# Kernel tuning notes

Measured on AMD Instinct MI355X. Metric: run time of the kernel, lower is better.

Reference implementation:

```python
import jax, jax.numpy as jnp
import numpy as np

N_NODES = 50000
N_EDGES = 800000
IN_FEATS = 128
NUM_HEADS = 4
OUT_FEATS = 32


def setup_inputs() -> dict:
    key = jax.random.key(0)
    k1, k2, k3, k4 = jax.random.split(key, 4)
    feat = jax.random.normal(k1, (N_NODES, IN_FEATS), dtype=jnp.float32)
    # nn.Linear weight: [out_features, in_features] = [H*D, in]
    W = jax.random.normal(k2, (NUM_HEADS * OUT_FEATS, IN_FEATS), dtype=jnp.float32) * (1.0 / np.sqrt(IN_FEATS))
    src = jax.random.randint(k3, (N_EDGES,), 0, N_NODES, dtype=jnp.int32)
    dst = jax.random.randint(k4, (N_EDGES,), 0, N_NODES, dtype=jnp.int32)
    return {"feat": feat, "W": W, "src": src, "dst": dst}


def reference(feat, W, src, dst):
    N = feat.shape[0]
    H, D = NUM_HEADS, OUT_FEATS
    scale = jnp.float32(1.0 / np.sqrt(D))
    # fc: feat @ W.T  ->  [N, H, D]
    ft = (feat @ W.T).reshape(N, H, D)
    ft_src = ft[src]                                   # [E, H, D] gather
    # u_dot_v: per-edge, per-head dot product, scaled by sqrt(out_feats)
    a = jnp.einsum('ehd,ehd->eh', ft_src, ft[dst]) * scale  # [E, H]
    # edge softmax normalized by destination node (numerically stable)
    m = jax.ops.segment_max(a, dst, num_segments=N)    # [N, H]
    e = jnp.exp(a - m[dst])                            # [E, H]
    s = jax.ops.segment_sum(e, dst, num_segments=N)    # [N, H]
    sa = e / s[dst]                                    # [E, H]
    # u_mul_e + sum aggregation: scatter-add weighted source features into dst
    out = jax.ops.segment_sum(ft_src * sa[:, :, None], dst, num_segments=N)  # [N, H, D]
    return out
```

## Files before the change

kernel.cpp:

```cpp
#include <hip/hip_runtime.h>
#include <math.h>

#define NN 50000
#define NE 800000
#define HH 4
#define DD 32

typedef __attribute__((ext_vector_type(8))) short short8;
typedef __attribute__((ext_vector_type(4))) float f32x4;

__device__ __forceinline__ unsigned short f2bf(float x) {
    unsigned u = __float_as_uint(x);
    unsigned r = (u + 0x7FFF + ((u >> 16) & 1)) >> 16;
    return (unsigned short)r;
}

__device__ __forceinline__ short8 pack8(float4 p, float4 q) {
    short8 r;
    r[0] = (short)f2bf(p.x); r[1] = (short)f2bf(p.y);
    r[2] = (short)f2bf(p.z); r[3] = (short)f2bf(p.w);
    r[4] = (short)f2bf(q.x); r[5] = (short)f2bf(q.y);
    r[6] = (short)f2bf(q.z); r[7] = (short)f2bf(q.w);
    return r;
}

__global__ __launch_bounds__(256) void k_gemm(const float* __restrict__ feat,
                                              const float* __restrict__ W,
                                              float* __restrict__ ft, int N) {
    __shared__ short8 wlds[2048];

    int tid = threadIdx.x;
#pragma unroll
    for (int j = 0; j < 8; ++j) {
        int f = tid + j * 256;
        int kc = f >> 9, ct = (f >> 6) & 7, l = f & 63;
        int o = ct * 16 + (l & 15);
        int kb = kc * 32 + ((l >> 4) << 3);
        const float* wp = W + o * 128 + kb;
        float4 p = *(const float4*)wp;
        float4 q = *(const float4*)(wp + 4);
        wlds[f] = pack8(p, q);
    }
    __syncthreads();

    int l = tid & 63;
    int w = tid >> 6;
    int row0 = blockIdx.x * 64;
    int arow = row0 + w * 16 + (l & 15);
    bool valid = arow < N;
    const float* fb = feat + (size_t)(valid ? arow : 0) * 128 + ((l >> 4) << 3);

    f32x4 acc[8];
#pragma unroll
    for (int ct = 0; ct < 8; ++ct) acc[ct] = (f32x4){0.f, 0.f, 0.f, 0.f};

#pragma unroll
    for (int kc = 0; kc < 4; ++kc) {
        short8 a;
        if (valid) {
            float4 p = *(const float4*)(fb + kc * 32);
            float4 q = *(const float4*)(fb + kc * 32 + 4);
            a = pack8(p, q);
        } else {
            a = (short8){0, 0, 0, 0, 0, 0, 0, 0};
        }
#pragma unroll
        for (int ct = 0; ct < 8; ++ct) {
            short8 b = wlds[kc * 512 + ct * 64 + l];
            acc[ct] = __builtin_amdgcn_mfma_f32_16x16x32_bf16(a, b, acc[ct], 0, 0, 0);
        }
    }

    int oc = l & 15;
    int rg = l >> 4;
#pragma unroll
    for (int i = 0; i < 4; ++i) {
        int r = row0 + w * 16 + rg * 4 + i;
        if (r < N) {
            float* op = ft + (size_t)r * 128 + oc;
#pragma unroll
            for (int ct = 0; ct < 8; ++ct) op[ct * 16] = acc[ct][i];
        }
    }
}

__global__ __launch_bounds__(256) void k_hist(const int* __restrict__ dst, int* __restrict__ cnt) {
    int e = blockIdx.x * 256 + threadIdx.x;
    if (e < NE) atomicAdd(&cnt[dst[e]], 1);
}

__global__ __launch_bounds__(256) void k_scan1(const int* __restrict__ cnt, int* __restrict__ row,
                                               int* __restrict__ partial, int n) {
    __shared__ int sh[256];
    int i = blockIdx.x * 256 + threadIdx.x;
    int x = (i < n) ? cnt[i] : 0;
    sh[threadIdx.x] = x;
    __syncthreads();
    for (int off = 1; off < 256; off <<= 1) {
        int v = (threadIdx.x >= off) ? sh[threadIdx.x - off] : 0;
        __syncthreads();
        sh[threadIdx.x] += v;
        __syncthreads();
    }
    if (i < n) row[i] = sh[threadIdx.x] - x;
    if (threadIdx.x == 255) partial[blockIdx.x] = sh[255];
}

__global__ __launch_bounds__(256) void k_scan2(int* __restrict__ partial, int nb) {
    __shared__ int sh[256];
    int t = threadIdx.x;
    int x = (t < nb) ? partial[t] : 0;
    sh[t] = x;
    __syncthreads();
    for (int off = 1; off < 256; off <<= 1) {
        int v = (t >= off) ? sh[t - off] : 0;
        __syncthreads();
        sh[t] += v;
        __syncthreads();
    }
    if (t < nb) partial[t] = sh[t] - x;
}

__global__ __launch_bounds__(256) void k_scan3(int* __restrict__ row, int* __restrict__ cur,
                                               const int* __restrict__ partial, int n) {
    int i = blockIdx.x * 256 + threadIdx.x;
    if (i < n) {
        int val = row[i] + partial[blockIdx.x];
        row[i] = val;
        cur[i] = val;
    }
    if (i == 0) row[n] = NE;
}

__global__ __launch_bounds__(256) void k_fill(const int* __restrict__ src, const int* __restrict__ dst,
                                              int* __restrict__ cur, int* __restrict__ srcs) {
    int e = blockIdx.x * 256 + threadIdx.x;
    if (e >= NE) return;
    int p = atomicAdd(&cur[dst[e]], 1);
    srcs[p] = src[e];
}

__global__ __launch_bounds__(256) void k_agg(const float2* __restrict__ ft2,
                                             const int* __restrict__ row,
                                             const int* __restrict__ srcs,
                                             float2* __restrict__ out2) {
    int n = blockIdx.x * 4 + (threadIdx.x >> 6);
    int l = threadIdx.x & 63;
    int r0 = row[n], r1 = row[n + 1];
    size_t base = (size_t)n * 64 + l;
    float2 fd = ft2[base];
    float m = -INFINITY, s = 0.f;
    float ax = 0.f, ay = 0.f;
    int p = r0;
    for (; p + 1 < r1; p += 2) {
        int s0 = srcs[p], s1 = srcs[p + 1];
        float2 f0 = ft2[(size_t)s0 * 64 + l];
        float2 f1 = ft2[(size_t)s1 * 64 + l];
        float v0 = fd.x * f0.x + fd.y * f0.y;
        float v1 = fd.x * f1.x + fd.y * f1.y;
        v0 += __shfl_xor(v0, 1);  v1 += __shfl_xor(v1, 1);
        v0 += __shfl_xor(v0, 2);  v1 += __shfl_xor(v1, 2);
        v0 += __shfl_xor(v0, 4);  v1 += __shfl_xor(v1, 4);
        v0 += __shfl_xor(v0, 8);  v1 += __shfl_xor(v1, 8);
        v0 *= 0.17677669529663687f;
        v1 *= 0.17677669529663687f;
        float mn = fmaxf(fmaxf(m, v0), v1);
        float sc = __expf(m - mn);
        float w0 = __expf(v0 - mn);
        float w1 = __expf(v1 - mn);
        s = s * sc + w0 + w1;
        ax = ax * sc + w0 * f0.x + w1 * f1.x;
        ay = ay * sc + w0 * f0.y + w1 * f1.y;
        m = mn;
    }
    if (p < r1) {
        int s0 = srcs[p];
        float2 f0 = ft2[(size_t)s0 * 64 + l];
        float v0 = fd.x * f0.x + fd.y * f0.y;
        v0 += __shfl_xor(v0, 1);
        v0 += __shfl_xor(v0, 2);
        v0 += __shfl_xor(v0, 4);
        v0 += __shfl_xor(v0, 8);
        v0 *= 0.17677669529663687f;
        float mn = fmaxf(m, v0);
        float sc = __expf(m - mn);
        float w0 = __expf(v0 - mn);
        s = s * sc + w0;
        ax = ax * sc + w0 * f0.x;
        ay = ay * sc + w0 * f0.y;
    }
    float inv = (r1 > r0) ? 1.f / s : 0.f;
    out2[base] = make_float2(ax * inv, ay * inv);
}

extern "C" void kernel_launch(void* const* d_in, const int* in_sizes, int n_in,
                              void* d_out, int out_size, void* d_ws, size_t ws_size,
                              hipStream_t stream) {
    const float* feat = (const float*)d_in[0];
    const float* W    = (const float*)d_in[1];
    const int*   src  = (const int*)d_in[2];
    const int*   dst  = (const int*)d_in[3];
    float* out = (float*)d_out;

    float* ft   = (float*)d_ws;
    int*   row  = (int*)(ft + (size_t)NN * 128);
    int*   cur  = row + (NN + 1);
    int*   srcs = cur + NN;
    int*   cnt  = srcs + NE;
    int*   part = cnt + NN;

    const int NB1 = (NN + 255) / 256;

    hipMemsetAsync(cnt, 0, (size_t)NN * sizeof(int), stream);
    k_hist<<<(NE + 255) / 256, 256, 0, stream>>>(dst, cnt);
    k_scan1<<<NB1, 256, 0, stream>>>(cnt, row, part, NN);
    k_scan2<<<1, 256, 0, stream>>>(part, NB1);
    k_scan3<<<NB1, 256, 0, stream>>>(row, cur, part, NN);
    k_fill<<<(NE + 255) / 256, 256, 0, stream>>>(src, dst, cur, srcs);

    k_gemm<<<(NN + 63) / 64, 256, 0, stream>>>(feat, W, ft, NN);
    k_agg<<<NN / 4, 256, 0, stream>>>((const float2*)ft, row, srcs, (float2*)out);
}
```

Before: 260.0 us.

## Fuse CSR build into one cooperative kernel with grid syncs

Replaces the five CSR-construction launches (histogram, three scan stages, fill) with a single cooperative kernel that uses grid-wide syncs between phases. The histogram's atomic return value is stored per edge as a position, so the fill phase writes directly to row[dst]+pos without a second atomic pass. The aim is to remove launch overhead and the second round of contended atomics. In exchange it adds an extra NE-sized workspace array and grid-sync costs, and it depends on all 2048 blocks being co-resident.

```diff
diff --git a/kernel.cpp b/kernel.cpp
--- a/kernel.cpp
+++ b/kernel.cpp
@@ -1,5 +1,8 @@
 #include <hip/hip_runtime.h>
+#include <hip/hip_cooperative_groups.h>
 #include <math.h>
+
+namespace cg = cooperative_groups;
 
 #define NN 50000
 #define NE 800000
@@ -84,60 +87,63 @@
     }
 }
 
-__global__ __launch_bounds__(256) void k_hist(const int* __restrict__ dst, int* __restrict__ cnt) {
-    int e = blockIdx.x * 256 + threadIdx.x;
-    if (e < NE) atomicAdd(&cnt[dst[e]], 1);
-}
-
-__global__ __launch_bounds__(256) void k_scan1(const int* __restrict__ cnt, int* __restrict__ row,
-                                               int* __restrict__ partial, int n) {
+__global__ __launch_bounds__(256, 8) void k_csr(const int* __restrict__ src,
+                                                const int* __restrict__ dst,
+                                                int* __restrict__ cnt,
+                                                int* __restrict__ pos,
+                                                int* __restrict__ row,
+                                                int* __restrict__ part,
+                                                int* __restrict__ srcs) {
+    cg::grid_group grid = cg::this_grid();
     __shared__ int sh[256];
-    int i = blockIdx.x * 256 + threadIdx.x;
-    int x = (i < n) ? cnt[i] : 0;
-    sh[threadIdx.x] = x;
-    __syncthreads();
-    for (int off = 1; off < 256; off <<= 1) {
-        int v = (threadIdx.x >= off) ? sh[threadIdx.x - off] : 0;
+    const int tid = threadIdx.x, bid = blockIdx.x;
+    const int nthr = gridDim.x * 256;
+    const int gtid = bid * 256 + tid;
+
+    for (int e = gtid; e < NE; e += nthr)
+        pos[e] = atomicAdd(&cnt[dst[e]], 1);
+    grid.sync();
+
+    const int NCH = (NN + 255) / 256;
+    if (bid < NCH) {
+        int i = bid * 256 + tid;
+        int x = (i < NN) ? cnt[i] : 0;
+        sh[tid] = x;
         __syncthreads();
-        sh[threadIdx.x] += v;
+        for (int off = 1; off < 256; off <<= 1) {
+            int v = (tid >= off) ? sh[tid - off] : 0;
+            __syncthreads();
+            sh[tid] += v;
+            __syncthreads();
+        }
+        if (i < NN) row[i] = sh[tid] - x;
+        if (tid == 255) part[bid] = sh[255];
+    }
+    grid.sync();
+
+    if (bid == 0) {
+        int x = (tid < NCH) ? part[tid] : 0;
+        sh[tid] = x;
         __syncthreads();
-    }
-    if (i < n) row[i] = sh[threadIdx.x] - x;
-    if (threadIdx.x == 255) partial[blockIdx.x] = sh[255];
-}
-
-__global__ __launch_bounds__(256) void k_scan2(int* __restrict__ partial, int nb) {
-    __shared__ int sh[256];
-    int t = threadIdx.x;
-    int x = (t < nb) ? partial[t] : 0;
-    sh[t] = x;
-    __syncthreads();
-    for (int off = 1; off < 256; off <<= 1) {
-        int v = (t >= off) ? sh[t - off] : 0;
-        __syncthreads();
-        sh[t] += v;
-        __syncthreads();
-    }
-    if (t < nb) partial[t] = sh[t] - x;
-}
-
-__global__ __launch_bounds__(256) void k_scan3(int* __restrict__ row, int* __restrict__ cur,
-                                               const int* __restrict__ partial, int n) {
-    int i = blockIdx.x * 256 + threadIdx.x;
-    if (i < n) {
-        int val = row[i] + partial[blockIdx.x];
-        row[i] = val;
-        cur[i] = val;
-    }
-    if (i == 0) row[n] = NE;
-}
-
-__global__ __launch_bounds__(256) void k_fill(const int* __restrict__ src, const int* __restrict__ dst,
-                                              int* __restrict__ cur, int* __restrict__ srcs) {
-    int e = blockIdx.x * 256 + threadIdx.x;
-    if (e >= NE) return;
-    int p = atomicAdd(&cur[dst[e]], 1);
-    srcs[p] = src[e];
+        for (int off = 1; off < 256; off <<= 1) {
+            int v = (tid >= off) ? sh[tid - off] : 0;
+            __syncthreads();
+            sh[tid] += v;
+            __syncthreads();
+        }
+        if (tid < NCH) part[tid] = sh[tid] - x;
+    }
+    grid.sync();
+
+    if (bid < NCH) {
+        int i = bid * 256 + tid;
+        if (i < NN) row[i] += part[bid];
+    }
+    if (gtid == 0) row[NN] = NE;
+    grid.sync();
+
+    for (int e = gtid; e < NE; e += nthr)
+        srcs[row[dst[e]] + pos[e]] = src[e];
 }
 
 __global__ __launch_bounds__(256) void k_agg(const float2* __restrict__ ft2,
@@ -204,20 +210,17 @@
 
     float* ft   = (float*)d_ws;
     int*   row  = (int*)(ft + (size_t)NN * 128);
-    int*   cur  = row + (NN + 1);
-    int*   srcs = cur + NN;
+    int*   pos  = row + (NN + 1);
+    int*   srcs = pos + NE;
     int*   cnt  = srcs + NE;
     int*   part = cnt + NN;
 
-    const int NB1 = (NN + 255) / 256;
-
     hipMemsetAsync(cnt, 0, (size_t)NN * sizeof(int), stream);
-    k_hist<<<(NE + 255) / 256, 256, 0, stream>>>(dst, cnt);
-    k_scan1<<<NB1, 256, 0, stream>>>(cnt, row, part, NN);
-    k_scan2<<<1, 256, 0, stream>>>(part, NB1);
-    k_scan3<<<NB1, 256, 0, stream>>>(row, cur, part, NN);
-    k_fill<<<(NE + 255) / 256, 256, 0, stream>>>(src, dst, cur, srcs);
-
     k_gemm<<<(NN + 63) / 64, 256, 0, stream>>>(feat, W, ft, NN);
+
+    void* args[] = {(void*)&src, (void*)&dst, (void*)&cnt, (void*)&pos,
+                    (void*)&row, (void*)&part, (void*)&srcs};
+    hipLaunchCooperativeKernel((void*)k_csr, dim3(2048), dim3(256), args, 0, stream);
+
     k_agg<<<NN / 4, 256, 0, stream>>>((const float2*)ft, row, srcs, (float2*)out);
 }
```

Measured after the change: 971.9 us. 3.74x slower.
